# Performance work log

Hardware: AMD Instinct MI355X
Metric: run time of the kernel (lower is better)

Reference implementation:

```python
import jax, jax.numpy as jnp
import numpy as np
from jax import lax

CLIP = 1.0  # STE clip value for both input and kernel quantizers
EPS = 1e-3  # keras BatchNormalization default epsilon

@jax.custom_vjp
def binarize(x):
    # sign with >=0 -> +1, <0 -> -1 (matches tf.where(x>=0, 1, -1))
    return jnp.where(x >= 0, jnp.ones_like(x), -jnp.ones_like(x))

def _bin_fwd(x):
    return binarize(x), x

def _bin_bwd(x, g):
    # straight-through estimator: pass grad where |x| <= clip, else 0
    return (jnp.where(jnp.abs(x) <= CLIP, g, jnp.zeros_like(g)),)

binarize.defvjp(_bin_fwd, _bin_bwd)

def setup_inputs() -> dict:
    key = jax.random.key(0)
    k1, k2, k3 = jax.random.split(key, 3)
    B, H, Wd, C = 32, 56, 56, 128
    x = jax.random.normal(k1, (B, H, Wd, C), dtype=jnp.float32)
    W = jax.random.normal(k2, (3, 3, C, C), dtype=jnp.float32) * 0.05  # HWIO
    gamma = jnp.ones((C,), dtype=jnp.float32) + 0.1 * jax.random.normal(k3, (C,), dtype=jnp.float32)
    beta = jnp.zeros((C,), dtype=jnp.float32)
    return {"x": x, "W": W, "gamma": gamma, "beta": beta}

def reference(x, W, gamma, beta):
    # binarize activations and weights (sign with STE grad)
    xb = binarize(x)
    wb = binarize(W)
    # 3x3 SAME conv, stride 1, NHWC / HWIO
    y = lax.conv_general_dilated(
        xb, wb, window_strides=(1, 1), padding='SAME',
        dimension_numbers=('NHWC', 'HWIO', 'NHWC'))
    r = jax.nn.relu(y)
    # training-mode batch norm over axes (0,1,2)
    mean = jnp.mean(r, axis=(0, 1, 2), keepdims=True)
    var = jnp.var(r, axis=(0, 1, 2), keepdims=True)
    r_std = (r - mean) * lax.rsqrt(var + EPS)
    out_bn = gamma * r_std + beta
    # shortcut add with (un-binarized) input
    return out_bn + x
```

## Files before the change

kernel.cpp:

```cpp
#include <hip/hip_runtime.h>

#define CH    128
#define HH    56
#define WW    56
#define BB    32
#define NPIX  (BB * HH * WW)
#define NSLOT 16

#define XROW   7424
#define XBATCH 430592
#define LDSROW 8448
#define SWZ(pl, ci) ((ci) ^ (((pl) & 7) << 4))

typedef int i32x4  __attribute__((ext_vector_type(4)));
typedef int i32x16 __attribute__((ext_vector_type(16)));

__device__ __forceinline__ void mfma_i8(i32x16& acc, i32x4 a, i32x4 b) {
    asm("v_mfma_i32_32x32x32_i8 %0, %1, %2, %0" : "+v"(acc) : "v"(a), "v"(b));
}

__global__ __launch_bounds__(256) void prep_k(const float* __restrict__ x,
                                              const float* __restrict__ Wt,
                                              signed char* __restrict__ xi8,
                                              signed char* __restrict__ wfrag,
                                              unsigned long long* __restrict__ accum) {
    int bx = blockIdx.x, tid = threadIdx.x;
    if (bx < 12544) {
        int t = bx * 256 + tid;
        int p = t >> 5;
        int ci0 = (t & 31) * 4;
        int w = p % WW;
        int t2 = p / WW;
        int h = t2 % HH;
        int b = t2 / HH;
        float4 v = ((const float4*)x)[t];
        unsigned o = (v.x >= 0.f ? 0x01u : 0xFFu)
                   | ((v.y >= 0.f ? 0x01u : 0xFFu) << 8)
                   | ((v.z >= 0.f ? 0x01u : 0xFFu) << 16)
                   | ((v.w >= 0.f ? 0x01u : 0xFFu) << 24);
        *(unsigned*)(xi8 + (size_t)b * XBATCH + (size_t)(h + 1) * XROW + (w + 1) * 128 + ci0) = o;
    } else if (bx < 12772) {
        int c = (bx - 12544) * 256 + tid;
        int cell = c >> 3, q = c & 7;
        int b = cell / 228, e = cell % 228;
        int row, col;
        if (e < 58)       { row = 0;       col = e; }
        else if (e < 116) { row = 57;      col = e - 58; }
        else if (e < 172) { row = e - 115; col = 0; }
        else              { row = e - 171; col = 57; }
        i32x4 z = {0, 0, 0, 0};
        *(i32x4*)(xi8 + (size_t)b * XBATCH + (size_t)row * XROW + col * 128 + q * 16) = z;
    } else if (bx < 12808) {
        int i = (bx - 12772) * 256 + tid;
        int n = i / 2304;
        int r = i % 2304;
        int q = r / 64;
        int L = r % 64;
        int tap = q >> 2, kk = q & 3;
        int co = 32 * n + (L & 31);
        int kbase = 32 * kk + (L >> 5) * 16;
        i32x4 o;
        #pragma unroll
        for (int d = 0; d < 4; ++d) {
            unsigned u = 0;
            #pragma unroll
            for (int by = 0; by < 4; ++by) {
                int ci = kbase + 4 * d + by;
                unsigned s = (Wt[((size_t)tap * 128 + ci) * 128 + co] >= 0.f) ? 0x01u : 0xFFu;
                u |= s << (8 * by);
            }
            o[d] = (int)u;
        }
        *(i32x4*)(wfrag + (size_t)i * 16) = o;
    } else {
        for (int k = tid; k < NSLOT * 256; k += 256) accum[k] = 0ull;
    }
}

__global__ __launch_bounds__(512) void gemm_k(const signed char* __restrict__ xi8,
                                              const signed char* __restrict__ wfrag,
                                              unsigned long long* __restrict__ accum,
                                              unsigned short* __restrict__ rb) {
    __shared__ alignas(16) char sm[4 * LDSROW];

    int ph0 = 1 + ((blockIdx.x * 7) % HH);
    int b   = (blockIdx.x * 7) / HH;

    int L = threadIdx.x & 63, w = threadIdx.x >> 6;
    int n32 = w & 3, sh = w >> 2;
    int l31 = L & 31, hi = L >> 5;

    int coff[3][4];
    #pragma unroll
    for (int dw = 0; dw < 3; ++dw) {
        int pld = l31 + dw;
        int pl = 32 * sh + pld;
        #pragma unroll
        for (int kk = 0; kk < 4; ++kk)
            coff[dw][kk] = pl * 128 + ((32 * kk + 16 * hi) ^ ((pld & 7) << 4));
    }

    const i32x4* bfp = (const i32x4*)wfrag + (size_t)n32 * 36 * 64;
    i32x4 bfr[36];
    #pragma unroll
    for (int q = 0; q < 36; ++q) bfr[q] = bfp[q * 64 + L];

    int co = 32 * n32 + l31;

    for (int c = threadIdx.x; c < 1392; c += 512) {
        int rr = c / 464;
        int off = (c % 464) * 16;
        int row = ph0 - 1 + rr;
        int p = off >> 7, ci0 = off & 127;
        i32x4 v = *(const i32x4*)(xi8 + (size_t)b * XBATCH + (size_t)row * XROW + off);
        int pl = p + 1;
        *(i32x4*)(sm + (row & 3) * LDSROW + pl * 128 + SWZ(pl, ci0)) = v;
    }
    if (threadIdx.x < 256) {
        int slot = threadIdx.x >> 6, g = threadIdx.x & 63;
        int gp = g >> 3, ci0 = (g & 7) * 16;
        int pl = (gp == 0) ? 0 : (58 + gp);
        i32x4 z = {0, 0, 0, 0};
        *(i32x4*)(sm + slot * LDSROW + pl * 128 + SWZ(pl, ci0)) = z;
    }
    __syncthreads();

    #pragma unroll 1
    for (int t = 0; t < 7; ++t) {
        int ph = ph0 + t;
        int id = blockIdx.x * 7 + t;

        i32x4 stv;
        int stdst = -1;
        if (t < 6 && threadIdx.x < 464) {
            int nrow = ph + 2;
            int off = threadIdx.x * 16;
            int p = off >> 7, ci0 = off & 127;
            stv = *(const i32x4*)(xi8 + (size_t)b * XBATCH + (size_t)nrow * XROW + off);
            int pl = p + 1;
            stdst = (nrow & 3) * LDSROW + pl * 128 + SWZ(pl, ci0);
        }

        int rs[3] = { ((ph - 1) & 3) * LDSROW, (ph & 3) * LDSROW, ((ph + 1) & 3) * LDSROW };

        i32x16 acc0 = {}, acc1 = {};
        #pragma unroll
        for (int q = 0; q < 36; ++q) {
            int tap = q >> 2, kk = q & 3;
            int dh = tap / 3, dw = tap % 3;
            i32x4 a = *(const i32x4*)(sm + rs[dh] + coff[dw][kk]);
            if (q & 1) mfma_i8(acc1, a, bfr[q]);
            else       mfma_i8(acc0, a, bfr[q]);
        }
        asm volatile("s_nop 7\n\ts_nop 7\n\ts_nop 7" : "+v"(acc0), "+v"(acc1));
        #pragma unroll
        for (int e = 0; e < 16; ++e) acc0[e] += acc1[e];

        unsigned s1 = 0, s2 = 0;
        size_t rbase = (((size_t)b * HH + (ph - 1)) * WW) * CH + co;
        #pragma unroll
        for (int reg = 0; reg < 16; ++reg) {
            int pw = 32 * sh + (reg & 3) + 8 * (reg >> 2) + 4 * hi;
            int y = acc0[reg];
            int r = y > 0 ? y : 0;
            if (pw >= 1 && pw <= WW) {
                s1 += (unsigned)r;
                s2 += (unsigned)__mul24(r, r);
                rb[rbase + (size_t)(pw - 1) * CH] = (unsigned short)r;
            }
        }
        s1 += __shfl_xor(s1, 32);
        s2 += __shfl_xor(s2, 32);
        if (hi == 0) {
            int slot = id & (NSLOT - 1);
            atomicAdd(&accum[slot * 256 + co],       (unsigned long long)s1);
            atomicAdd(&accum[slot * 256 + 128 + co], (unsigned long long)s2);
        }

        if (stdst >= 0) *(i32x4*)(sm + stdst) = stv;

        __syncthreads();
    }
}

__global__ __launch_bounds__(256) void out_k(const unsigned short* __restrict__ rb,
                                             const unsigned long long* __restrict__ accum,
                                             const float* __restrict__ gamma,
                                             const float* __restrict__ beta,
                                             const float* __restrict__ x,
                                             float* __restrict__ out) {
    __shared__ float2 ssl[CH];
    int tid = threadIdx.x;
    if (tid < CH) {
        unsigned long long a1 = 0, a2 = 0;
        #pragma unroll
        for (int s = 0; s < NSLOT; ++s) {
            a1 += accum[s * 256 + tid];
            a2 += accum[s * 256 + 128 + tid];
        }
        float N    = (float)NPIX;
        float mean = (float)a1 / N;
        float ex2  = (float)a2 / N;
        float var  = fmaf(-mean, mean, ex2);
        float rstd = 1.0f / sqrtf(var + 1e-3f);
        float sc   = gamma[tid] * rstd;
        float2 v;
        v.x = sc;
        v.y = fmaf(-mean, sc, beta[tid]);
        ssl[tid] = v;
    }
    __syncthreads();

    int c4 = tid & 31;
    float2 s0 = ssl[c4 * 4 + 0], s1 = ssl[c4 * 4 + 1];
    float2 s2 = ssl[c4 * 4 + 2], s3 = ssl[c4 * 4 + 3];
    int base = blockIdx.x * 2048 + tid;
    #pragma unroll
    for (int k = 0; k < 8; ++k) {
        int idx4 = base + k * 256;
        ushort4 r = ((const ushort4*)rb)[idx4];
        float4 xv = ((const float4*)x)[idx4];
        float4 o;
        o.x = fmaf((float)r.x, s0.x, s0.y + xv.x);
        o.y = fmaf((float)r.y, s1.x, s1.y + xv.y);
        o.z = fmaf((float)r.z, s2.x, s2.y + xv.z);
        o.w = fmaf((float)r.w, s3.x, s3.y + xv.w);
        ((float4*)out)[idx4] = o;
    }
}

extern "C" void kernel_launch(void* const* d_in, const int* in_sizes, int n_in,
                              void* d_out, int out_size, void* d_ws, size_t ws_size,
                              hipStream_t stream) {
    const float* x     = (const float*)d_in[0];
    const float* Wt    = (const float*)d_in[1];
    const float* gamma = (const float*)d_in[2];
    const float* beta  = (const float*)d_in[3];
    float* out = (float*)d_out;
    char* ws = (char*)d_ws;

    signed char* xi8   = (signed char*)ws;
    signed char* wfrag = (signed char*)(ws + 13778944);
    unsigned long long* accum = (unsigned long long*)(ws + 13926400);
    unsigned short* rb = (unsigned short*)(ws + 13959168);

    hipLaunchKernelGGL(prep_k, dim3(12809), dim3(256), 0, stream, x, Wt, xi8, wfrag, accum);
    hipLaunchKernelGGL(gemm_k, dim3(256), dim3(512), 0, stream, xi8, wfrag, accum, rb);
    hipLaunchKernelGGL(out_k,  dim3(NPIX * CH / 4 / 2048), dim3(256), 0, stream,
                       rb, accum, gamma, beta, x, out);
}
```

Before: 60.43 us.

## Recompute binary conv in second pass instead of storing ReLU intermediate

Replaces the store-then-normalize scheme with two passes over the int8 MFMA convolution. The first pass only accumulates per-channel sum and sum of squares. The second recomputes the convolution and applies batch norm plus the residual directly to the output. This removes writing and re-reading the 16-bit ReLU buffer, at the cost of doubling the MFMA work and LDS staging. The fused epilogue also writes scalar floats in a strided per-lane pattern rather than float4, which may coalesce less well.

```diff
diff --git a/kernel.cpp b/kernel.cpp
--- a/kernel.cpp
+++ b/kernel.cpp
@@ -77,10 +77,9 @@
     }
 }
 
-__global__ __launch_bounds__(512) void gemm_k(const signed char* __restrict__ xi8,
-                                              const signed char* __restrict__ wfrag,
-                                              unsigned long long* __restrict__ accum,
-                                              unsigned short* __restrict__ rb) {
+__global__ __launch_bounds__(512) void gemm1_k(const signed char* __restrict__ xi8,
+                                               const signed char* __restrict__ wfrag,
+                                               unsigned long long* __restrict__ accum) {
     __shared__ alignas(16) char sm[4 * LDSROW];
 
     int ph0 = 1 + ((blockIdx.x * 7) % HH);
@@ -157,7 +156,6 @@
         for (int e = 0; e < 16; ++e) acc0[e] += acc1[e];
 
         unsigned s1 = 0, s2 = 0;
-        size_t rbase = (((size_t)b * HH + (ph - 1)) * WW) * CH + co;
         #pragma unroll
         for (int reg = 0; reg < 16; ++reg) {
             int pw = 32 * sh + (reg & 3) + 8 * (reg >> 2) + 4 * hi;
@@ -166,7 +164,6 @@
             if (pw >= 1 && pw <= WW) {
                 s1 += (unsigned)r;
                 s2 += (unsigned)__mul24(r, r);
-                rb[rbase + (size_t)(pw - 1) * CH] = (unsigned short)r;
             }
         }
         s1 += __shfl_xor(s1, 32);
@@ -178,54 +175,127 @@
         }
 
         if (stdst >= 0) *(i32x4*)(sm + stdst) = stv;
-
         __syncthreads();
     }
 }
 
-__global__ __launch_bounds__(256) void out_k(const unsigned short* __restrict__ rb,
-                                             const unsigned long long* __restrict__ accum,
-                                             const float* __restrict__ gamma,
-                                             const float* __restrict__ beta,
-                                             const float* __restrict__ x,
-                                             float* __restrict__ out) {
+__global__ __launch_bounds__(512) void gemm2_k(const signed char* __restrict__ xi8,
+                                               const signed char* __restrict__ wfrag,
+                                               const unsigned long long* __restrict__ accum,
+                                               const float* __restrict__ gamma,
+                                               const float* __restrict__ beta,
+                                               const float* __restrict__ x,
+                                               float* __restrict__ out) {
+    __shared__ alignas(16) char sm[4 * LDSROW];
     __shared__ float2 ssl[CH];
-    int tid = threadIdx.x;
-    if (tid < CH) {
+
+    int ph0 = 1 + ((blockIdx.x * 7) % HH);
+    int b   = (blockIdx.x * 7) / HH;
+
+    int L = threadIdx.x & 63, w = threadIdx.x >> 6;
+    int n32 = w & 3, sh = w >> 2;
+    int l31 = L & 31, hi = L >> 5;
+
+    int coff[3][4];
+    #pragma unroll
+    for (int dw = 0; dw < 3; ++dw) {
+        int pld = l31 + dw;
+        int pl = 32 * sh + pld;
+        #pragma unroll
+        for (int kk = 0; kk < 4; ++kk)
+            coff[dw][kk] = pl * 128 + ((32 * kk + 16 * hi) ^ ((pld & 7) << 4));
+    }
+
+    const i32x4* bfp = (const i32x4*)wfrag + (size_t)n32 * 36 * 64;
+    i32x4 bfr[36];
+    #pragma unroll
+    for (int q = 0; q < 36; ++q) bfr[q] = bfp[q * 64 + L];
+
+    int co = 32 * n32 + l31;
+
+    for (int c = threadIdx.x; c < 1392; c += 512) {
+        int rr = c / 464;
+        int off = (c % 464) * 16;
+        int row = ph0 - 1 + rr;
+        int p = off >> 7, ci0 = off & 127;
+        i32x4 v = *(const i32x4*)(xi8 + (size_t)b * XBATCH + (size_t)row * XROW + off);
+        int pl = p + 1;
+        *(i32x4*)(sm + (row & 3) * LDSROW + pl * 128 + SWZ(pl, ci0)) = v;
+    }
+    if (threadIdx.x < 256) {
+        int slot = threadIdx.x >> 6, g = threadIdx.x & 63;
+        int gp = g >> 3, ci0 = (g & 7) * 16;
+        int pl = (gp == 0) ? 0 : (58 + gp);
+        i32x4 z = {0, 0, 0, 0};
+        *(i32x4*)(sm + slot * LDSROW + pl * 128 + SWZ(pl, ci0)) = z;
+    }
+    if (threadIdx.x < CH) {
+        int c = threadIdx.x;
         unsigned long long a1 = 0, a2 = 0;
         #pragma unroll
         for (int s = 0; s < NSLOT; ++s) {
-            a1 += accum[s * 256 + tid];
-            a2 += accum[s * 256 + 128 + tid];
+            a1 += accum[s * 256 + c];
+            a2 += accum[s * 256 + 128 + c];
         }
         float N    = (float)NPIX;
         float mean = (float)a1 / N;
         float ex2  = (float)a2 / N;
         float var  = fmaf(-mean, mean, ex2);
         float rstd = 1.0f / sqrtf(var + 1e-3f);
-        float sc   = gamma[tid] * rstd;
+        float sc   = gamma[c] * rstd;
         float2 v;
         v.x = sc;
-        v.y = fmaf(-mean, sc, beta[tid]);
-        ssl[tid] = v;
+        v.y = fmaf(-mean, sc, beta[c]);
+        ssl[c] = v;
     }
     __syncthreads();
 
-    int c4 = tid & 31;
-    float2 s0 = ssl[c4 * 4 + 0], s1 = ssl[c4 * 4 + 1];
-    float2 s2 = ssl[c4 * 4 + 2], s3 = ssl[c4 * 4 + 3];
-    int base = blockIdx.x * 2048 + tid;
-    #pragma unroll
-    for (int k = 0; k < 8; ++k) {
-        int idx4 = base + k * 256;
-        ushort4 r = ((const ushort4*)rb)[idx4];
-        float4 xv = ((const float4*)x)[idx4];
-        float4 o;
-        o.x = fmaf((float)r.x, s0.x, s0.y + xv.x);
-        o.y = fmaf((float)r.y, s1.x, s1.y + xv.y);
-        o.z = fmaf((float)r.z, s2.x, s2.y + xv.z);
-        o.w = fmaf((float)r.w, s3.x, s3.y + xv.w);
-        ((float4*)out)[idx4] = o;
+    float2 ss = ssl[co];
+
+    #pragma unroll 1
+    for (int t = 0; t < 7; ++t) {
+        int ph = ph0 + t;
+
+        i32x4 stv;
+        int stdst = -1;
+        if (t < 6 && threadIdx.x < 464) {
+            int nrow = ph + 2;
+            int off = threadIdx.x * 16;
+            int p = off >> 7, ci0 = off & 127;
+            stv = *(const i32x4*)(xi8 + (size_t)b * XBATCH + (size_t)nrow * XROW + off);
+            int pl = p + 1;
+            stdst = (nrow & 3) * LDSROW + pl * 128 + SWZ(pl, ci0);
+        }
+
+        int rs[3] = { ((ph - 1) & 3) * LDSROW, (ph & 3) * LDSROW, ((ph + 1) & 3) * LDSROW };
+
+        i32x16 acc0 = {}, acc1 = {};
+        #pragma unroll
+        for (int q = 0; q < 36; ++q) {
+            int tap = q >> 2, kk = q & 3;
+            int dh = tap / 3, dw = tap % 3;
+            i32x4 a = *(const i32x4*)(sm + rs[dh] + coff[dw][kk]);
+            if (q & 1) mfma_i8(acc1, a, bfr[q]);
+            else       mfma_i8(acc0, a, bfr[q]);
+        }
+        asm volatile("s_nop 7\n\ts_nop 7\n\ts_nop 7" : "+v"(acc0), "+v"(acc1));
+        #pragma unroll
+        for (int e = 0; e < 16; ++e) acc0[e] += acc1[e];
+
+        size_t obase = (((size_t)b * HH + (ph - 1)) * WW) * CH + co;
+        #pragma unroll
+        for (int reg = 0; reg < 16; ++reg) {
+            int pw = 32 * sh + (reg & 3) + 8 * (reg >> 2) + 4 * hi;
+            int y = acc0[reg];
+            float r = (float)(y > 0 ? y : 0);
+            if (pw >= 1 && pw <= WW) {
+                size_t idx = obase + (size_t)(pw - 1) * CH;
+                out[idx] = fmaf(r, ss.x, ss.y + x[idx]);
+            }
+        }
+
+        if (stdst >= 0) *(i32x4*)(sm + stdst) = stv;
+        __syncthreads();
     }
 }
 
@@ -242,10 +312,9 @@
     signed char* xi8   = (signed char*)ws;
     signed char* wfrag = (signed char*)(ws + 13778944);
     unsigned long long* accum = (unsigned long long*)(ws + 13926400);
-    unsigned short* rb = (unsigned short*)(ws + 13959168);
-
-    hipLaunchKernelGGL(prep_k, dim3(12809), dim3(256), 0, stream, x, Wt, xi8, wfrag, accum);
-    hipLaunchKernelGGL(gemm_k, dim3(256), dim3(512), 0, stream, xi8, wfrag, accum, rb);
-    hipLaunchKernelGGL(out_k,  dim3(NPIX * CH / 4 / 2048), dim3(256), 0, stream,
-                       rb, accum, gamma, beta, x, out);
-}
+
+    hipLaunchKernelGGL(prep_k,  dim3(12809), dim3(256), 0, stream, x, Wt, xi8, wfrag, accum);
+    hipLaunchKernelGGL(gemm1_k, dim3(256),   dim3(512), 0, stream, xi8, wfrag, accum);
+    hipLaunchKernelGGL(gemm2_k, dim3(256),   dim3(512), 0, stream, xi8, wfrag, accum,
+                       gamma, beta, x, out);
+}
```

After: 86.59 us. 1.43x slower.
